# Kernel tuning notes

Measured on AMD Instinct MI355X. Metric: run time of the kernel, lower is better.

## Reference

```python
import jax, jax.numpy as jnp
import numpy as np

# ---- static config (from init_kwargs) ----
SAMPLE_RATE = 2048.0
MAX_SHIFT = int(0.025 * SAMPLE_RATE)          # 51 samples
NUM_BINS = 16
FFTLENGTH = 1.0                               # chisq_kernel_length (s)
DF = 1.0 / FFTLENGTH
NUM_FREQS = int(FFTLENGTH * SAMPLE_RATE // 2 + 1)   # 1025 == rfft bins of 2048 samples
HIGHPASS = 32.0
CHISQ_PENALTY = 1.0
_freqs = np.arange(NUM_FREQS) / FFTLENGTH
MASK = _freqs >= HIGHPASS                     # static numpy bool mask

BATCH, CHANNELS, DIM = 256, 2, 2048


def setup_inputs() -> dict:
    key = jax.random.key(0)
    k1, k2 = jax.random.split(key)
    x_hat = jax.random.normal(k1, (BATCH, CHANNELS, DIM), dtype=jnp.float32)
    x = jax.random.normal(k2, (BATCH, CHANNELS, DIM), dtype=jnp.float32)
    return {"x_hat": x_hat, "x": x}


def _center(x):
    xmin = x.min(-1, keepdims=True)
    xmax = x.max(-1, keepdims=True)
    return 2 * (x - xmin) / (xmax - xmin) - 1


def _shifted_pearson(x, y, max_shift):
    # x, y: [B, C, T]; returns corr: [W, B, C] with W = 2*max_shift + 1
    b, c, t = x.shape
    num_windows = 2 * max_shift + 1
    xp = jnp.pad(x, ((0, 0), (0, 0), (max_shift, max_shift)))
    # window w, position i -> xp[..., i + w]  (same layout as torch unfold)
    idx = jnp.arange(num_windows)[:, None] + jnp.arange(t)[None, :]   # [W, T]
    xw = xp[:, :, idx]                                                # [B, C, W, T]
    xw = jnp.transpose(xw, (2, 0, 1, 3))                              # [W, B, C, T]
    xw = xw - xw.mean(-1, keepdims=True)
    yc = y - y.mean(-1, keepdims=True)
    corr = (xw * yc).sum(-1)
    norm = (xw ** 2).sum(-1) * (yc ** 2).sum(-1)
    return corr / jnp.sqrt(norm)


def _snr_integral(a, b):
    # |4 * a * conj(b) * df| cumulatively summed over frequency
    integrand = a * jnp.conj(b)
    return jnp.abs(4 * integrand * DF).cumsum(-1)


def _chisq(htilde, stilde):
    htilde = htilde[:, :, MASK]
    stilde = stilde[:, :, MASK]
    # partition frequencies by the template's own optimal-SNR integral
    si = _snr_integral(htilde, htilde)                    # [B, C, F]
    total = si[:, :, -1:]
    bins = (jnp.arange(NUM_BINS + 1, dtype=si.dtype) / NUM_BINS) * total  # [B, C, NB+1]
    search = jax.vmap(jax.vmap(lambda a, v: jnp.searchsorted(a, v, side="right")))
    edges = search(si, bins)
    edges = jnp.clip(edges, 0, si.shape[-1] - 1)
    qtilde = htilde / jnp.sqrt(total).astype(htilde.dtype)
    # SNR per bin of the normalized template against the strain
    si2 = _snr_integral(qtilde, stilde)                   # [B, C, F]
    total2 = si2[:, :, -1:]
    right = jnp.take_along_axis(si2, edges[:, :, 1:], axis=-1)
    left = jnp.take_along_axis(si2, edges[:, :, :-1], axis=-1)
    snr_per_bin = right - left                            # [B, C, NB]
    summand = (snr_per_bin - total2 / NUM_BINS) ** 2
    chisq = NUM_BINS * summand.sum(-1) / (NUM_BINS - 1)
    return total2[:, :, 0], chisq


def reference(x_hat, x):
    x_hat = _center(x_hat)
    corr = _shifted_pearson(x_hat, x, MAX_SHIFT)          # [W, B, C]
    corr = corr.max(0)                                    # [B, C]
    loss = (1 - corr) / (1 + corr)
    htilde = jnp.fft.rfft(x_hat, axis=-1) / SAMPLE_RATE   # [B, C, 1025] complex
    stilde = jnp.fft.rfft(x, axis=-1) / SAMPLE_RATE
    _, chisq = _chisq(htilde, stilde)
    chisq = chisq * CHISQ_PENALTY
    loss = loss * (1 + chisq ** 3) ** (1.0 / 6.0)
    return loss
```

## Files before the change

kernel.cpp:

```cpp
#include <hip/hip_runtime.h>
#include <math.h>

#define ROWS 512
#define DIM 2048
#define MS 51
#define NWIN 103
#define KMIN 32
#define NMASK 993
#define INVS (1.0f/8192.0f)

__global__ __launch_bounds__(512) void fused_mfl_kernel(
    const float* __restrict__ xhat, const float* __restrict__ x,
    float* __restrict__ out)
{
    const int r = blockIdx.x;
    const int t = threadIdx.x;
    const int lane = t & 63;
    const int wave = t >> 6;
    const float* xh = xhat + (size_t)r * DIM;
    const float* xr = x + (size_t)r * DIM;

    __shared__ float smem[11780];
    float2* A  = (float2*)smem;
    float2* Bb = (float2*)(smem + 4096);
    float2* TW = (float2*)(smem + 8192);
    float* red6  = smem;
    float* siA   = smem + 9216;
    float* siBr  = smem + 10240;
    float* headS = smem + 11264;
    float* headQ = smem + 11316;
    float* tailS = smem + 11368;
    float* tailQ = smem + 11420;
    float* yhH   = smem + 11472;
    float* yhT   = smem + 11523;
    float* ycH   = smem + 11574;
    float* ycT   = smem + 11625;
    float* corrv = smem + 11676;

    __shared__ float sc[8];
    __shared__ int   edges[17];
    __shared__ float summ[16];
    __shared__ float wsA[8], wsB[8];

    float4 a4 = ((const float4*)xh)[t];
    float4 b4 = ((const float4*)xr)[t];
    float av[4] = {a4.x, a4.y, a4.z, a4.w};
    float bv[4] = {b4.x, b4.y, b4.z, b4.w};

    {
        float swv, cwv;
        sincosf((float)t * (-3.14159265358979323846f / 1024.0f), &swv, &cwv);
        TW[t] = make_float2(cwv, swv);
    }

    auto fft_stage = [&](const float2* Sp, float2* Dp, const int s) {
        const int q = t;
        const int u = q & ~(s - 1);
        float2 x0 = Sp[q];
        float2 x1 = Sp[q + 512];
        float2 x2 = Sp[q + 1024];
        float2 x3 = Sp[q + 1536];
        float t0r = x0.x + x2.x, t0i = x0.y + x2.y;
        float t1r = x0.x - x2.x, t1i = x0.y - x2.y;
        float t2r = x1.x + x3.x, t2i = x1.y + x3.y;
        float d3r = x1.x - x3.x, d3i = x1.y - x3.y;
        float t3r = d3i, t3i = -d3r;
        float2 w1 = TW[u];
        float w2r = w1.x * w1.x - w1.y * w1.y, w2i = 2.f * w1.x * w1.y;
        float w3r = w2r * w1.x - w2i * w1.y,  w3i = w2r * w1.y + w2i * w1.x;
        float y0r = t0r + t2r, y0i = t0i + t2i;
        float a1r = t1r + t3r, a1i = t1i + t3i;
        float y1r = a1r * w1.x - a1i * w1.y, y1i = a1r * w1.y + a1i * w1.x;
        float a2r = t0r - t2r, a2i = t0i - t2i;
        float y2r = a2r * w2r - a2i * w2i, y2i = a2r * w2i + a2i * w2r;
        float a3r = t1r - t3r, a3i = t1i - t3i;
        float y3r = a3r * w3r - a3i * w3i, y3i = a3r * w3i + a3i * w3r;
        int base = q + 3 * u;
        Dp[base]         = make_float2(y0r, y0i);
        Dp[base + s]     = make_float2(y1r, y1i);
        Dp[base + 2 * s] = make_float2(y2r, y2i);
        Dp[base + 3 * s] = make_float2(y3r, y3i);
    };

    {
        float mn4 = fminf(fminf(av[0], av[1]), fminf(av[2], av[3]));
        float mx4 = fmaxf(fmaxf(av[0], av[1]), fmaxf(av[2], av[3]));
        float sa = (av[0] + av[1]) + (av[2] + av[3]);
        float qa = (av[0]*av[0] + av[1]*av[1]) + (av[2]*av[2] + av[3]*av[3]);
        float sx = (bv[0] + bv[1]) + (bv[2] + bv[3]);
        float qx = (bv[0]*bv[0] + bv[1]*bv[1]) + (bv[2]*bv[2] + bv[3]*bv[3]);
        red6[t]        = mn4;
        red6[512 + t]  = mx4;
        red6[1024 + t] = sa;
        red6[1536 + t] = qa;
        red6[2048 + t] = sx;
        red6[2560 + t] = qx;
    }
    __syncthreads();
    if (wave == 0) {
        float4 u, v;
        u = ((const float4*)(red6       ))[2*lane]; v = ((const float4*)(red6       ))[2*lane+1];
        float pmn = fminf(fminf(fminf(u.x,u.y),fminf(u.z,u.w)),
                          fminf(fminf(v.x,v.y),fminf(v.z,v.w)));
        u = ((const float4*)(red6 +  512))[2*lane]; v = ((const float4*)(red6 +  512))[2*lane+1];
        float pmx = fmaxf(fmaxf(fmaxf(u.x,u.y),fmaxf(u.z,u.w)),
                          fmaxf(fmaxf(v.x,v.y),fmaxf(v.z,v.w)));
        u = ((const float4*)(red6 + 1024))[2*lane]; v = ((const float4*)(red6 + 1024))[2*lane+1];
        float psa = ((u.x+u.y)+(u.z+u.w)) + ((v.x+v.y)+(v.z+v.w));
        u = ((const float4*)(red6 + 1536))[2*lane]; v = ((const float4*)(red6 + 1536))[2*lane+1];
        float pqa = ((u.x+u.y)+(u.z+u.w)) + ((v.x+v.y)+(v.z+v.w));
        u = ((const float4*)(red6 + 2048))[2*lane]; v = ((const float4*)(red6 + 2048))[2*lane+1];
        float psx = ((u.x+u.y)+(u.z+u.w)) + ((v.x+v.y)+(v.z+v.w));
        u = ((const float4*)(red6 + 2560))[2*lane]; v = ((const float4*)(red6 + 2560))[2*lane+1];
        float pqx = ((u.x+u.y)+(u.z+u.w)) + ((v.x+v.y)+(v.z+v.w));
#pragma unroll
        for (int d = 32; d; d >>= 1) {
            pmn = fminf(pmn, __shfl_down(pmn, d));
            pmx = fmaxf(pmx, __shfl_down(pmx, d));
            psa += __shfl_down(psa, d);
            pqa += __shfl_down(pqa, d);
            psx += __shfl_down(psx, d);
            pqx += __shfl_down(pqx, d);
        }
        if (lane == 0) {
            float mn = pmn, mx = pmx;
            float scl = 2.0f / (mx - mn);
            float mean = psx * (1.0f / DIM);
            float Sm = psa - (float)DIM * mn;
            float S1v = scl * Sm - (float)DIM;
            float S2v = scl * scl * (pqa - 2.f * mn * psa + (float)DIM * mn * mn)
                      - 2.f * scl * Sm + (float)DIM;
            float Syyv = pqx - (float)DIM * mean * mean;
            sc[0] = mn; sc[1] = scl; sc[2] = mean;
            sc[3] = S1v; sc[4] = S2v; sc[5] = Syyv;
        }
    }
    __syncthreads();
    const float mnv = sc[0], scl = sc[1], mean = sc[2];
    const float S1 = sc[3], S2 = sc[4], Syy = sc[5];

#pragma unroll
    for (int j = 0; j < 4; ++j) {
        int i = 4 * t + j;
        float y = (av[j] - mnv) * scl - 1.0f;
        float z = bv[j] - mean;
        A[i] = make_float2(y, bv[j]);
        if (i < MS)        { yhH[i] = y;        ycH[i] = z; }
        if (i >= DIM - MS) { yhT[i - (DIM - MS)] = y; ycT[i - (DIM - MS)] = z; }
    }
    __syncthreads();

    if (wave < 2) {
        float v = 0.f;
        if (lane >= 1 && lane <= MS)
            v = (wave == 0) ? yhH[lane - 1] : yhT[MS - lane];
        float s = v, q = v * v;
#pragma unroll
        for (int d = 1; d < 64; d <<= 1) {
            float ys = __shfl_up(s, d);
            float yq = __shfl_up(q, d);
            if (lane >= d) { s += ys; q += yq; }
        }
        if (lane <= MS) {
            if (wave == 0) { headS[lane] = s; headQ[lane] = q; }
            else           { tailS[lane] = s; tailQ[lane] = q; }
        }
    }

    fft_stage(A, Bb, 1);    __syncthreads();
    fft_stage(Bb, A, 4);    __syncthreads();
    fft_stage(A, Bb, 16);   __syncthreads();
    fft_stage(Bb, A, 64);   __syncthreads();
    fft_stage(A, Bb, 256);  __syncthreads();

    const float MSC = 0.5f * (1.0f / 2048.0f);
    float h[2], sg[2];
#pragma unroll
    for (int j = 0; j < 2; ++j) {
        int m = 2 * t + j;
        if (m < NMASK) {
            int f = m + KMIN;
            float zfr, zfi;
            if (f < 1024) {
                float2 p = Bb[f], q2 = Bb[f + 1024];
                zfr = p.x + q2.x; zfi = p.y + q2.y;
            } else {
                float2 p = Bb[0], q2 = Bb[1024];
                zfr = p.x - q2.x; zfi = p.y - q2.y;
            }
            int g = 2048 - f;
            float2 p2 = Bb[g - 1024], q3 = Bb[g];
            float zgr = p2.x - q3.x, zgi = p2.y - q3.y;
            float hre = zfr + zgr, him = zfi - zgi;
            float sre = zfi + zgi, sim = zgr - zfr;
            h[j]  = sqrtf(hre * hre + him * him) * MSC;
            sg[j] = sqrtf(sre * sre + sim * sim) * MSC;
            float pr = hre * sre + him * sim;
            float pi = him * sre - hre * sim;
            A[f] = make_float2(pr, -pi);
            if (f < 1024) A[2048 - f] = make_float2(pr, pi);
        } else { h[j] = 0.f; sg[j] = 0.f; }
    }
    if (t < 32) {
        if (t == 0) A[0] = make_float2(0.f, 0.f);
        else {
            int f = t;
            float2 p = Bb[f], q2 = Bb[f + 1024];
            float zfr = p.x + q2.x, zfi = p.y + q2.y;
            float2 p2 = Bb[1024 - f], q3 = Bb[2048 - f];
            float zgr = p2.x - q3.x, zgi = p2.y - q3.y;
            float hre = zfr + zgr, him = zfi - zgi;
            float sre = zfi + zgi, sim = zgr - zfr;
            float pr = hre * sre + him * sim;
            float pi = him * sre - hre * sim;
            A[f] = make_float2(pr, -pi);
            A[2048 - f] = make_float2(pr, pi);
        }
    }
    __syncthreads();

    float e0 = 4.f * h[0] * h[0];
    float e1 = e0 + 4.f * h[1] * h[1];
    float g0 = 4.f * h[0] * sg[0];
    float g1 = g0 + 4.f * h[1] * sg[1];
    float totE = e1, totG = g1;
    float incE = totE, incG = totG;
#pragma unroll
    for (int d = 1; d < 64; d <<= 1) {
        float yE = __shfl_up(incE, d);
        float yG = __shfl_up(incG, d);
        if (lane >= d) { incE += yE; incG += yG; }
    }
    if (lane == 63) { wsA[wave] = incE; wsB[wave] = incG; }
    fft_stage(A, Bb, 1);
    __syncthreads();

    {
        float offE = 0.f, offG = 0.f;
        for (int w = 0; w < wave; ++w) { offE += wsA[w]; offG += wsB[w]; }
        float preE = offE + incE - totE;
        float preG = offG + incG - totG;
        siA[2 * t]      = preE + e0;
        siA[2 * t + 1]  = preE + e1;
        siBr[2 * t]     = preG + g0;
        siBr[2 * t + 1] = preG + g1;
    }
    fft_stage(Bb, A, 4);
    __syncthreads();

    const float total  = siA[NMASK - 1];
    const float qf     = 1.0f / sqrtf(total);
    const float total2 = siBr[NMASK - 1] * qf;
    if (t < 17) {
        float bin = ((float)t * (1.0f / 16.0f)) * total;
        int lo = 0, hi = NMASK;
        while (lo < hi) {
            int mid = (lo + hi) >> 1;
            if (siA[mid] <= bin) lo = mid + 1; else hi = mid;
        }
        edges[t] = (lo < NMASK - 1) ? lo : (NMASK - 1);
    }
    fft_stage(A, Bb, 16);
    __syncthreads();

    if (t < 16) {
        float snr = (siBr[edges[t + 1]] - siBr[edges[t]]) * qf;
        float d = snr - total2 * (1.0f / 16.0f);
        summ[t] = d * d;
    }
    fft_stage(Bb, A, 64);
    __syncthreads();

    fft_stage(A, Bb, 256);
    __syncthreads();

    if (t < 4 * NWIN) {
        int c = t >> 2, k = t & 3;
        int off = c - MS;
        float acc = 0.f;
        if (off > 0) {
            for (int j = k; j < off; j += 4) acc += yhH[j] * ycT[MS - off + j];
        } else if (off < 0) {
            for (int j = k; j < -off; j += 4) acc += yhT[MS + off + j] * ycH[j];
        }
        acc += __shfl_down(acc, 1);
        acc += __shfl_down(acc, 2);
        if (k == 0) {
            int sidx = (off >= 0) ? off : (2048 + off);
            float cc = (sidx < 1024) ? (Bb[sidx].x + Bb[sidx + 1024].x)
                                     : (Bb[sidx - 1024].x - Bb[sidx].x);
            float num = cc * INVS - acc;
            float sw, qw;
            if (off >= 0) { sw = S1 - headS[off];  qw = S2 - headQ[off]; }
            else          { sw = S1 - tailS[-off]; qw = S2 - tailQ[-off]; }
            float varw = qw - sw * sw * (1.0f / DIM);
            corrv[c] = num / sqrtf(varw * Syy);
        }
    }
    __syncthreads();

    if (wave == 0) {
        float m = (lane < NWIN) ? corrv[lane] : -2.0f;
        if (lane + 64 < NWIN) m = fmaxf(m, corrv[lane + 64]);
#pragma unroll
        for (int d = 32; d; d >>= 1) m = fmaxf(m, __shfl_down(m, d));
        if (lane == 0) {
            float loss0 = (1.0f - m) / (1.0f + m);
            float ssum = 0.f;
            for (int i = 0; i < 16; ++i) ssum += summ[i];
            float chisq = 16.0f * ssum / 15.0f;
            float c3 = chisq * chisq * chisq;
            out[r] = loss0 * powf(1.0f + c3, 1.0f / 6.0f);
        }
    }
}

extern "C" void kernel_launch(void* const* d_in, const int* in_sizes, int n_in,
                              void* d_out, int out_size, void* d_ws, size_t ws_size,
                              hipStream_t stream) {
    const float* xhat = (const float*)d_in[0];
    const float* x    = (const float*)d_in[1];
    float* out = (float*)d_out;
    (void)in_sizes; (void)n_in; (void)out_size; (void)d_ws; (void)ws_size;

    fused_mfl_kernel<<<ROWS, 512, 0, stream>>>(xhat, x, out);
}
```

Measured before the change: 68.43 us.

## Run forward FFT on raw inputs and use half-size inverse FFT for real correlation

The forward FFT now runs on the raw x_hat/x values rather than the centered signal. The min/max scaling is folded algebraically into the correlation numerator and window variance, which removes a barrier and the centering pass before the FFT. The inverse FFT of the real cross-spectrum is replaced by a 1024-point complex FFT on 256 threads, using a packed real-output trick. The remaining 256 threads do the SNR prefix scans and binning concurrently. This cuts FFT work and overlaps the chisq bookkeeping, at the cost of more intricate algebra with possible precision differences and idle threads during the half-size stages.

After: 67.72 us. Within noise of the previous version (-1.0%).

```diff
diff --git a/kernel.cpp b/kernel.cpp
--- a/kernel.cpp
+++ b/kernel.cpp
@@ -7,7 +7,6 @@
 #define NWIN 103
 #define KMIN 32
 #define NMASK 993
-#define INVS (1.0f/8192.0f)
 
 __global__ __launch_bounds__(512) void fused_mfl_kernel(
     const float* __restrict__ xhat, const float* __restrict__ x,
@@ -17,33 +16,37 @@
     const int t = threadIdx.x;
     const int lane = t & 63;
     const int wave = t >> 6;
-    const float* xh = xhat + (size_t)r * DIM;
-    const float* xr = x + (size_t)r * DIM;
-
-    __shared__ float smem[11780];
-    float2* A  = (float2*)smem;
-    float2* Bb = (float2*)(smem + 4096);
-    float2* TW = (float2*)(smem + 8192);
-    float* red6  = smem;
-    float* siA   = smem + 9216;
-    float* siBr  = smem + 10240;
-    float* headS = smem + 11264;
-    float* headQ = smem + 11316;
-    float* tailS = smem + 11368;
-    float* tailQ = smem + 11420;
-    float* yhH   = smem + 11472;
-    float* yhT   = smem + 11523;
-    float* ycH   = smem + 11574;
-    float* ycT   = smem + 11625;
-    float* corrv = smem + 11676;
+
+    __shared__ float smem[12928];
+    float2* A2  = (float2*)smem;
+    float2* B2  = (float2*)(smem + 4096);
+    float2* TW  = (float2*)(smem + 8192);
+    float* eArr = smem + 9216;
+    float* gArr = smem + 10240;
+    float* red6 = smem + 9216;
+    float* ah   = smem + 12288;
+    float* xhd  = smem + 12339;
+    float* at_  = smem + 12390;
+    float* xt_  = smem + 12441;
+    float* Ah   = smem + 12492;
+    float* Aqh  = smem + 12544;
+    float* Xh   = smem + 12596;
+    float* At   = smem + 12648;
+    float* Aqt  = smem + 12700;
+    float* Xt   = smem + 12752;
+    float* corrv= smem + 12804;
+    float* siA  = smem;
+    float* siBr = smem + 1024;
 
     __shared__ float sc[8];
     __shared__ int   edges[17];
     __shared__ float summ[16];
-    __shared__ float wsA[8], wsB[8];
-
-    float4 a4 = ((const float4*)xh)[t];
-    float4 b4 = ((const float4*)xr)[t];
+    __shared__ float wsA[4], wsB[4];
+
+    const float* xhp = xhat + (size_t)r * DIM;
+    const float* xrp = x    + (size_t)r * DIM;
+    float4 a4 = ((const float4*)xhp)[t];
+    float4 b4 = ((const float4*)xrp)[t];
     float av[4] = {a4.x, a4.y, a4.z, a4.w};
     float bv[4] = {b4.x, b4.y, b4.z, b4.w};
 
@@ -53,225 +56,270 @@
         TW[t] = make_float2(cwv, swv);
     }
 
-    auto fft_stage = [&](const float2* Sp, float2* Dp, const int s) {
+#pragma unroll
+    for (int j = 0; j < 4; ++j) {
+        int i = 4 * t + j;
+        A2[i] = make_float2(av[j], bv[j]);
+        if (i < MS)        { ah[i] = av[j]; xhd[i] = bv[j]; }
+        if (i >= DIM - MS) { at_[i-(DIM-MS)] = av[j]; xt_[i-(DIM-MS)] = bv[j]; }
+    }
+    {
+        float mn4 = fminf(fminf(av[0],av[1]), fminf(av[2],av[3]));
+        float mx4 = fmaxf(fmaxf(av[0],av[1]), fmaxf(av[2],av[3]));
+        float sa = (av[0]+av[1])+(av[2]+av[3]);
+        float qa = (av[0]*av[0]+av[1]*av[1])+(av[2]*av[2]+av[3]*av[3]);
+        float sx = (bv[0]+bv[1])+(bv[2]+bv[3]);
+        float qx = (bv[0]*bv[0]+bv[1]*bv[1])+(bv[2]*bv[2]+bv[3]*bv[3]);
+        red6[t] = mn4; red6[512+t] = mx4; red6[1024+t] = sa;
+        red6[1536+t] = qa; red6[2048+t] = sx; red6[2560+t] = qx;
+    }
+    __syncthreads();
+
+    auto fft2048 = [&](const float2* Sp, float2* Dp, const int s) {
         const int q = t;
         const int u = q & ~(s - 1);
-        float2 x0 = Sp[q];
-        float2 x1 = Sp[q + 512];
-        float2 x2 = Sp[q + 1024];
-        float2 x3 = Sp[q + 1536];
-        float t0r = x0.x + x2.x, t0i = x0.y + x2.y;
-        float t1r = x0.x - x2.x, t1i = x0.y - x2.y;
-        float t2r = x1.x + x3.x, t2i = x1.y + x3.y;
-        float d3r = x1.x - x3.x, d3i = x1.y - x3.y;
-        float t3r = d3i, t3i = -d3r;
+        float2 x0 = Sp[q], x1 = Sp[q+512], x2 = Sp[q+1024], x3 = Sp[q+1536];
+        float t0r=x0.x+x2.x, t0i=x0.y+x2.y;
+        float t1r=x0.x-x2.x, t1i=x0.y-x2.y;
+        float t2r=x1.x+x3.x, t2i=x1.y+x3.y;
+        float d3r=x1.x-x3.x, d3i=x1.y-x3.y;
+        float t3r=d3i, t3i=-d3r;
         float2 w1 = TW[u];
-        float w2r = w1.x * w1.x - w1.y * w1.y, w2i = 2.f * w1.x * w1.y;
-        float w3r = w2r * w1.x - w2i * w1.y,  w3i = w2r * w1.y + w2i * w1.x;
-        float y0r = t0r + t2r, y0i = t0i + t2i;
-        float a1r = t1r + t3r, a1i = t1i + t3i;
-        float y1r = a1r * w1.x - a1i * w1.y, y1i = a1r * w1.y + a1i * w1.x;
-        float a2r = t0r - t2r, a2i = t0i - t2i;
-        float y2r = a2r * w2r - a2i * w2i, y2i = a2r * w2i + a2i * w2r;
-        float a3r = t1r - t3r, a3i = t1i - t3i;
-        float y3r = a3r * w3r - a3i * w3i, y3i = a3r * w3i + a3i * w3r;
-        int base = q + 3 * u;
-        Dp[base]         = make_float2(y0r, y0i);
-        Dp[base + s]     = make_float2(y1r, y1i);
-        Dp[base + 2 * s] = make_float2(y2r, y2i);
-        Dp[base + 3 * s] = make_float2(y3r, y3i);
+        float w2r=w1.x*w1.x-w1.y*w1.y, w2i=2.f*w1.x*w1.y;
+        float w3r=w2r*w1.x-w2i*w1.y,  w3i=w2r*w1.y+w2i*w1.x;
+        float y0r=t0r+t2r, y0i=t0i+t2i;
+        float a1r=t1r+t3r, a1i=t1i+t3i;
+        float y1r=a1r*w1.x-a1i*w1.y, y1i=a1r*w1.y+a1i*w1.x;
+        float a2r=t0r-t2r, a2i=t0i-t2i;
+        float y2r=a2r*w2r-a2i*w2i, y2i=a2r*w2i+a2i*w2r;
+        float a3r=t1r-t3r, a3i=t1i-t3i;
+        float y3r=a3r*w3r-a3i*w3i, y3i=a3r*w3i+a3i*w3r;
+        int base = q + 3*u;
+        Dp[base]       = make_float2(y0r,y0i);
+        Dp[base+s]     = make_float2(y1r,y1i);
+        Dp[base+2*s]   = make_float2(y2r,y2i);
+        Dp[base+3*s]   = make_float2(y3r,y3i);
     };
-
-    {
-        float mn4 = fminf(fminf(av[0], av[1]), fminf(av[2], av[3]));
-        float mx4 = fmaxf(fmaxf(av[0], av[1]), fmaxf(av[2], av[3]));
-        float sa = (av[0] + av[1]) + (av[2] + av[3]);
-        float qa = (av[0]*av[0] + av[1]*av[1]) + (av[2]*av[2] + av[3]*av[3]);
-        float sx = (bv[0] + bv[1]) + (bv[2] + bv[3]);
-        float qx = (bv[0]*bv[0] + bv[1]*bv[1]) + (bv[2]*bv[2] + bv[3]*bv[3]);
-        red6[t]        = mn4;
-        red6[512 + t]  = mx4;
-        red6[1024 + t] = sa;
-        red6[1536 + t] = qa;
-        red6[2048 + t] = sx;
-        red6[2560 + t] = qx;
-    }
-    __syncthreads();
+    auto fft1024 = [&](const float2* Sp, float2* Dp, const int s) {
+        const int q = t;
+        const int u = q & ~(s - 1);
+        float2 x0 = Sp[q], x1 = Sp[q+256], x2 = Sp[q+512], x3 = Sp[q+768];
+        float t0r=x0.x+x2.x, t0i=x0.y+x2.y;
+        float t1r=x0.x-x2.x, t1i=x0.y-x2.y;
+        float t2r=x1.x+x3.x, t2i=x1.y+x3.y;
+        float d3r=x1.x-x3.x, d3i=x1.y-x3.y;
+        float t3r=d3i, t3i=-d3r;
+        float2 w1 = TW[2*u];
+        float w2r=w1.x*w1.x-w1.y*w1.y, w2i=2.f*w1.x*w1.y;
+        float w3r=w2r*w1.x-w2i*w1.y,  w3i=w2r*w1.y+w2i*w1.x;
+        float y0r=t0r+t2r, y0i=t0i+t2i;
+        float a1r=t1r+t3r, a1i=t1i+t3i;
+        float y1r=a1r*w1.x-a1i*w1.y, y1i=a1r*w1.y+a1i*w1.x;
+        float a2r=t0r-t2r, a2i=t0i-t2i;
+        float y2r=a2r*w2r-a2i*w2i, y2i=a2r*w2i+a2i*w2r;
+        float a3r=t1r-t3r, a3i=t1i-t3i;
+        float y3r=a3r*w3r-a3i*w3i, y3i=a3r*w3i+a3i*w3r;
+        int base = q + 3*u;
+        Dp[base]       = make_float2(y0r,y0i);
+        Dp[base+s]     = make_float2(y1r,y1i);
+        Dp[base+2*s]   = make_float2(y2r,y2i);
+        Dp[base+3*s]   = make_float2(y3r,y3i);
+    };
+
+    fft2048(A2, B2, 1);
     if (wave == 0) {
         float4 u, v;
-        u = ((const float4*)(red6       ))[2*lane]; v = ((const float4*)(red6       ))[2*lane+1];
-        float pmn = fminf(fminf(fminf(u.x,u.y),fminf(u.z,u.w)),
-                          fminf(fminf(v.x,v.y),fminf(v.z,v.w)));
-        u = ((const float4*)(red6 +  512))[2*lane]; v = ((const float4*)(red6 +  512))[2*lane+1];
-        float pmx = fmaxf(fmaxf(fmaxf(u.x,u.y),fmaxf(u.z,u.w)),
-                          fmaxf(fmaxf(v.x,v.y),fmaxf(v.z,v.w)));
-        u = ((const float4*)(red6 + 1024))[2*lane]; v = ((const float4*)(red6 + 1024))[2*lane+1];
-        float psa = ((u.x+u.y)+(u.z+u.w)) + ((v.x+v.y)+(v.z+v.w));
-        u = ((const float4*)(red6 + 1536))[2*lane]; v = ((const float4*)(red6 + 1536))[2*lane+1];
-        float pqa = ((u.x+u.y)+(u.z+u.w)) + ((v.x+v.y)+(v.z+v.w));
-        u = ((const float4*)(red6 + 2048))[2*lane]; v = ((const float4*)(red6 + 2048))[2*lane+1];
-        float psx = ((u.x+u.y)+(u.z+u.w)) + ((v.x+v.y)+(v.z+v.w));
-        u = ((const float4*)(red6 + 2560))[2*lane]; v = ((const float4*)(red6 + 2560))[2*lane+1];
-        float pqx = ((u.x+u.y)+(u.z+u.w)) + ((v.x+v.y)+(v.z+v.w));
+        u=((const float4*)(red6     ))[2*lane]; v=((const float4*)(red6     ))[2*lane+1];
+        float pmn=fminf(fminf(fminf(u.x,u.y),fminf(u.z,u.w)),fminf(fminf(v.x,v.y),fminf(v.z,v.w)));
+        u=((const float4*)(red6+ 512))[2*lane]; v=((const float4*)(red6+ 512))[2*lane+1];
+        float pmx=fmaxf(fmaxf(fmaxf(u.x,u.y),fmaxf(u.z,u.w)),fmaxf(fmaxf(v.x,v.y),fmaxf(v.z,v.w)));
+        u=((const float4*)(red6+1024))[2*lane]; v=((const float4*)(red6+1024))[2*lane+1];
+        float psa=((u.x+u.y)+(u.z+u.w))+((v.x+v.y)+(v.z+v.w));
+        u=((const float4*)(red6+1536))[2*lane]; v=((const float4*)(red6+1536))[2*lane+1];
+        float pqa=((u.x+u.y)+(u.z+u.w))+((v.x+v.y)+(v.z+v.w));
+        u=((const float4*)(red6+2048))[2*lane]; v=((const float4*)(red6+2048))[2*lane+1];
+        float psx=((u.x+u.y)+(u.z+u.w))+((v.x+v.y)+(v.z+v.w));
+        u=((const float4*)(red6+2560))[2*lane]; v=((const float4*)(red6+2560))[2*lane+1];
+        float pqx=((u.x+u.y)+(u.z+u.w))+((v.x+v.y)+(v.z+v.w));
 #pragma unroll
         for (int d = 32; d; d >>= 1) {
-            pmn = fminf(pmn, __shfl_down(pmn, d));
-            pmx = fmaxf(pmx, __shfl_down(pmx, d));
-            psa += __shfl_down(psa, d);
-            pqa += __shfl_down(pqa, d);
-            psx += __shfl_down(psx, d);
-            pqx += __shfl_down(pqx, d);
+            pmn=fminf(pmn,__shfl_down(pmn,d)); pmx=fmaxf(pmx,__shfl_down(pmx,d));
+            psa+=__shfl_down(psa,d); pqa+=__shfl_down(pqa,d);
+            psx+=__shfl_down(psx,d); pqx+=__shfl_down(pqx,d);
         }
         if (lane == 0) {
-            float mn = pmn, mx = pmx;
-            float scl = 2.0f / (mx - mn);
-            float mean = psx * (1.0f / DIM);
-            float Sm = psa - (float)DIM * mn;
-            float S1v = scl * Sm - (float)DIM;
-            float S2v = scl * scl * (pqa - 2.f * mn * psa + (float)DIM * mn * mn)
-                      - 2.f * scl * Sm + (float)DIM;
-            float Syyv = pqx - (float)DIM * mean * mean;
-            sc[0] = mn; sc[1] = scl; sc[2] = mean;
-            sc[3] = S1v; sc[4] = S2v; sc[5] = Syyv;
-        }
-    }
-    __syncthreads();
-    const float mnv = sc[0], scl = sc[1], mean = sc[2];
-    const float S1 = sc[3], S2 = sc[4], Syy = sc[5];
-
-#pragma unroll
-    for (int j = 0; j < 4; ++j) {
-        int i = 4 * t + j;
-        float y = (av[j] - mnv) * scl - 1.0f;
-        float z = bv[j] - mean;
-        A[i] = make_float2(y, bv[j]);
-        if (i < MS)        { yhH[i] = y;        ycH[i] = z; }
-        if (i >= DIM - MS) { yhT[i - (DIM - MS)] = y; ycT[i - (DIM - MS)] = z; }
-    }
-    __syncthreads();
-
-    if (wave < 2) {
-        float v = 0.f;
-        if (lane >= 1 && lane <= MS)
-            v = (wave == 0) ? yhH[lane - 1] : yhT[MS - lane];
-        float s = v, q = v * v;
+            float scl = 2.0f/(pmx - pmn);
+            float Cc  = scl*pmn + 1.0f;
+            float mean = psx * (1.0f/DIM);
+            sc[0]=scl; sc[1]=Cc; sc[2]=mean; sc[3]=psa; sc[4]=pqa;
+            sc[5]=pqx - (float)DIM*mean*mean;
+        }
+    }
+    __syncthreads();
+
+    fft2048(B2, A2, 4);
+    if (wave == 2) {
+        float va=0.f, vq=0.f, vx=0.f;
+        if (lane >= 1 && lane <= MS) { float aa=ah[lane-1]; va=aa; vq=aa*aa; vx=xhd[lane-1]; }
 #pragma unroll
         for (int d = 1; d < 64; d <<= 1) {
-            float ys = __shfl_up(s, d);
-            float yq = __shfl_up(q, d);
-            if (lane >= d) { s += ys; q += yq; }
-        }
-        if (lane <= MS) {
-            if (wave == 0) { headS[lane] = s; headQ[lane] = q; }
-            else           { tailS[lane] = s; tailQ[lane] = q; }
-        }
-    }
-
-    fft_stage(A, Bb, 1);    __syncthreads();
-    fft_stage(Bb, A, 4);    __syncthreads();
-    fft_stage(A, Bb, 16);   __syncthreads();
-    fft_stage(Bb, A, 64);   __syncthreads();
-    fft_stage(A, Bb, 256);  __syncthreads();
+            float ya=__shfl_up(va,d), yq=__shfl_up(vq,d), yx=__shfl_up(vx,d);
+            if (lane >= d) { va+=ya; vq+=yq; vx+=yx; }
+        }
+        if (lane <= MS) { Ah[lane]=va; Aqh[lane]=vq; Xh[lane]=vx; }
+    } else if (wave == 3) {
+        float va=0.f, vq=0.f, vx=0.f;
+        if (lane >= 1 && lane <= MS) { float aa=at_[MS-lane]; va=aa; vq=aa*aa; vx=xt_[MS-lane]; }
+#pragma unroll
+        for (int d = 1; d < 64; d <<= 1) {
+            float ya=__shfl_up(va,d), yq=__shfl_up(vq,d), yx=__shfl_up(vx,d);
+            if (lane >= d) { va+=ya; vq+=yq; vx+=yx; }
+        }
+        if (lane <= MS) { At[lane]=va; Aqt[lane]=vq; Xt[lane]=vx; }
+    }
+    __syncthreads();
+    fft2048(A2, B2, 16);  __syncthreads();
+    fft2048(B2, A2, 64);  __syncthreads();
+    fft2048(A2, B2, 256); __syncthreads();
+
+    const float scl = sc[0], Cc = sc[1], mean = sc[2];
+    const float Sa = sc[3], Qa = sc[4], Szz = sc[5];
 
     const float MSC = 0.5f * (1.0f / 2048.0f);
-    float h[2], sg[2];
 #pragma unroll
     for (int j = 0; j < 2; ++j) {
         int m = 2 * t + j;
+        float e = 0.f, g = 0.f;
         if (m < NMASK) {
             int f = m + KMIN;
             float zfr, zfi;
-            if (f < 1024) {
-                float2 p = Bb[f], q2 = Bb[f + 1024];
-                zfr = p.x + q2.x; zfi = p.y + q2.y;
-            } else {
-                float2 p = Bb[0], q2 = Bb[1024];
-                zfr = p.x - q2.x; zfi = p.y - q2.y;
-            }
-            int g = 2048 - f;
-            float2 p2 = Bb[g - 1024], q3 = Bb[g];
+            if (f < 1024) { float2 p=B2[f], q2=B2[f+1024]; zfr=p.x+q2.x; zfi=p.y+q2.y; }
+            else          { float2 p=B2[0], q2=B2[1024];   zfr=p.x-q2.x; zfi=p.y-q2.y; }
+            int gi = 2048 - f;
+            float2 p2 = B2[gi-1024], q3 = B2[gi];
             float zgr = p2.x - q3.x, zgi = p2.y - q3.y;
             float hre = zfr + zgr, him = zfi - zgi;
             float sre = zfi + zgi, sim = zgr - zfr;
-            h[j]  = sqrtf(hre * hre + him * him) * MSC;
-            sg[j] = sqrtf(sre * sre + sim * sim) * MSC;
-            float pr = hre * sre + him * sim;
-            float pi = him * sre - hre * sim;
-            A[f] = make_float2(pr, -pi);
-            if (f < 1024) A[2048 - f] = make_float2(pr, pi);
-        } else { h[j] = 0.f; sg[j] = 0.f; }
+            float hm = scl * sqrtf(hre*hre + him*him) * MSC;
+            float sm = sqrtf(sre*sre + sim*sim) * MSC;
+            e = 4.f*hm*hm; g = 4.f*hm*sm;
+            float pr = hre*sre + him*sim;
+            float pi = him*sre - hre*sim;
+            A2[f] = make_float2(pr, -pi);
+            if (f < 1024) A2[2048-f] = make_float2(pr, pi);
+        }
+        eArr[m] = e; gArr[m] = g;
     }
     if (t < 32) {
-        if (t == 0) A[0] = make_float2(0.f, 0.f);
+        if (t == 0) A2[0] = make_float2(0.f, 0.f);
         else {
             int f = t;
-            float2 p = Bb[f], q2 = Bb[f + 1024];
-            float zfr = p.x + q2.x, zfi = p.y + q2.y;
-            float2 p2 = Bb[1024 - f], q3 = Bb[2048 - f];
-            float zgr = p2.x - q3.x, zgi = p2.y - q3.y;
-            float hre = zfr + zgr, him = zfi - zgi;
-            float sre = zfi + zgi, sim = zgr - zfr;
-            float pr = hre * sre + him * sim;
-            float pi = him * sre - hre * sim;
-            A[f] = make_float2(pr, -pi);
-            A[2048 - f] = make_float2(pr, pi);
-        }
-    }
-    __syncthreads();
-
-    float e0 = 4.f * h[0] * h[0];
-    float e1 = e0 + 4.f * h[1] * h[1];
-    float g0 = 4.f * h[0] * sg[0];
-    float g1 = g0 + 4.f * h[1] * sg[1];
-    float totE = e1, totG = g1;
-    float incE = totE, incG = totG;
-#pragma unroll
-    for (int d = 1; d < 64; d <<= 1) {
-        float yE = __shfl_up(incE, d);
-        float yG = __shfl_up(incG, d);
-        if (lane >= d) { incE += yE; incG += yG; }
-    }
-    if (lane == 63) { wsA[wave] = incE; wsB[wave] = incG; }
-    fft_stage(A, Bb, 1);
-    __syncthreads();
-
-    {
-        float offE = 0.f, offG = 0.f;
-        for (int w = 0; w < wave; ++w) { offE += wsA[w]; offG += wsB[w]; }
+            float2 p=B2[f], q2=B2[f+1024];
+            float zfr=p.x+q2.x, zfi=p.y+q2.y;
+            float2 p2=B2[1024-f], q3=B2[2048-f];
+            float zgr=p2.x-q3.x, zgi=p2.y-q3.y;
+            float hre=zfr+zgr, him=zfi-zgi;
+            float sre=zfi+zgi, sim=zgr-zfr;
+            float pr=hre*sre+him*sim, pi=him*sre-hre*sim;
+            A2[f]=make_float2(pr,-pi);
+            A2[2048-f]=make_float2(pr,pi);
+        }
+    }
+    __syncthreads();
+
+    float2* Qlo = B2;
+    float2* Qhi = B2 + 1024;
+
+    float se0=0,se1=0,se2=0,se3=0, sg0=0,sg1=0,sg2=0,sg3=0;
+    float incE=0, incG=0, totE=0, totG=0;
+
+    if (t < 256) {
+        const int q = t;
+        float2 wA = TW[q], wB = TW[q+256];
+        auto mkQ = [&](int k, float2 w, int ni) -> float2 {
+            float2 Pa = A2[k], Pb = A2[k+1024];
+            float D1r = Pa.x+Pb.x, D1i = Pa.y+Pb.y;
+            float D2r = Pa.x-Pb.x, D2i = Pa.y-Pb.y;
+            float Er = D2r*w.x - D2i*w.y;
+            float Ei = D2r*w.y + D2i*w.x;
+            if (ni) return make_float2(D1r - Er, D1i - Ei);
+            return make_float2(D1r + Ei, D1i - Er);
+        };
+        float2 x0 = mkQ(q,     wA, 0);
+        float2 x1 = mkQ(q+256, wB, 0);
+        float2 x2 = mkQ(q+512, wA, 1);
+        float2 x3 = mkQ(q+768, wB, 1);
+        float t0r=x0.x+x2.x, t0i=x0.y+x2.y;
+        float t1r=x0.x-x2.x, t1i=x0.y-x2.y;
+        float t2r=x1.x+x3.x, t2i=x1.y+x3.y;
+        float d3r=x1.x-x3.x, d3i=x1.y-x3.y;
+        float t3r=d3i, t3i=-d3r;
+        float2 w1 = TW[2*q];
+        float w2r=w1.x*w1.x-w1.y*w1.y, w2i=2.f*w1.x*w1.y;
+        float w3r=w2r*w1.x-w2i*w1.y,  w3i=w2r*w1.y+w2i*w1.x;
+        float y0r=t0r+t2r, y0i=t0i+t2i;
+        float a1r=t1r+t3r, a1i=t1i+t3i;
+        float y1r=a1r*w1.x-a1i*w1.y, y1i=a1r*w1.y+a1i*w1.x;
+        float a2r=t0r-t2r, a2i=t0i-t2i;
+        float y2r=a2r*w2r-a2i*w2i, y2i=a2r*w2i+a2i*w2r;
+        float a3r=t1r-t3r, a3i=t1i-t3i;
+        float y3r=a3r*w3r-a3i*w3i, y3i=a3r*w3i+a3i*w3r;
+        Qlo[4*q]   = make_float2(y0r,y0i);
+        Qlo[4*q+1] = make_float2(y1r,y1i);
+        Qlo[4*q+2] = make_float2(y2r,y2i);
+        Qlo[4*q+3] = make_float2(y3r,y3i);
+    } else {
+        int tt = t - 256;
+        float4 e4 = ((const float4*)eArr)[tt];
+        float4 g4 = ((const float4*)gArr)[tt];
+        se0=e4.x; se1=se0+e4.y; se2=se1+e4.z; se3=se2+e4.w;
+        sg0=g4.x; sg1=sg0+g4.y; sg2=sg1+g4.z; sg3=sg2+g4.w;
+        totE=se3; totG=sg3; incE=totE; incG=totG;
+#pragma unroll
+        for (int d = 1; d < 64; d <<= 1) {
+            float yE=__shfl_up(incE,d), yG=__shfl_up(incG,d);
+            if (lane >= d) { incE+=yE; incG+=yG; }
+        }
+        if (lane == 63) { wsA[wave-4]=incE; wsB[wave-4]=incG; }
+    }
+    __syncthreads();
+
+    if (t < 256) { fft1024(Qlo, Qhi, 4); }
+    else {
+        int tt = t - 256, w4 = wave - 4;
+        float offE=0.f, offG=0.f;
+        for (int w = 0; w < w4; ++w) { offE+=wsA[w]; offG+=wsB[w]; }
         float preE = offE + incE - totE;
         float preG = offG + incG - totG;
-        siA[2 * t]      = preE + e0;
-        siA[2 * t + 1]  = preE + e1;
-        siBr[2 * t]     = preG + g0;
-        siBr[2 * t + 1] = preG + g1;
-    }
-    fft_stage(Bb, A, 4);
-    __syncthreads();
-
-    const float total  = siA[NMASK - 1];
-    const float qf     = 1.0f / sqrtf(total);
-    const float total2 = siBr[NMASK - 1] * qf;
-    if (t < 17) {
-        float bin = ((float)t * (1.0f / 16.0f)) * total;
+        ((float4*)siA)[tt]  = make_float4(preE+se0, preE+se1, preE+se2, preE+se3);
+        ((float4*)siBr)[tt] = make_float4(preG+sg0, preG+sg1, preG+sg2, preG+sg3);
+    }
+    __syncthreads();
+
+    if (t < 256) { fft1024(Qhi, Qlo, 16); }
+    else if (t < 256 + 17) {
+        int tl = t - 256;
+        float total = siA[NMASK-1];
+        float bin = ((float)tl * (1.0f/16.0f)) * total;
         int lo = 0, hi = NMASK;
-        while (lo < hi) {
-            int mid = (lo + hi) >> 1;
-            if (siA[mid] <= bin) lo = mid + 1; else hi = mid;
-        }
-        edges[t] = (lo < NMASK - 1) ? lo : (NMASK - 1);
-    }
-    fft_stage(A, Bb, 16);
-    __syncthreads();
-
-    if (t < 16) {
-        float snr = (siBr[edges[t + 1]] - siBr[edges[t]]) * qf;
-        float d = snr - total2 * (1.0f / 16.0f);
-        summ[t] = d * d;
-    }
-    fft_stage(Bb, A, 64);
-    __syncthreads();
-
-    fft_stage(A, Bb, 256);
+        while (lo < hi) { int mid=(lo+hi)>>1; if (siA[mid] <= bin) lo=mid+1; else hi=mid; }
+        edges[tl] = (lo < NMASK-1) ? lo : (NMASK-1);
+    }
+    __syncthreads();
+
+    if (t < 256) { fft1024(Qlo, Qhi, 64); }
+    else if (t < 256 + 16) {
+        int tl = t - 256;
+        float total = siA[NMASK-1];
+        float qf = 1.0f / sqrtf(total);
+        float total2 = siBr[NMASK-1] * qf;
+        float snr = (siBr[edges[tl+1]] - siBr[edges[tl]]) * qf;
+        float d = snr - total2 * (1.0f/16.0f);
+        summ[tl] = d * d;
+    }
+    __syncthreads();
+
+    if (t < 256) { fft1024(Qhi, Qlo, 256); }
     __syncthreads();
 
     if (t < 4 * NWIN) {
@@ -279,38 +327,48 @@
         int off = c - MS;
         float acc = 0.f;
         if (off > 0) {
-            for (int j = k; j < off; j += 4) acc += yhH[j] * ycT[MS - off + j];
+            for (int j = k; j < off; j += 4) acc += ah[j] * (xt_[MS-off+j] - mean);
         } else if (off < 0) {
-            for (int j = k; j < -off; j += 4) acc += yhT[MS + off + j] * ycH[j];
+            int o = -off;
+            for (int j = k; j < o; j += 4) acc += at_[MS-o+j] * (xhd[j] - mean);
         }
         acc += __shfl_down(acc, 1);
         acc += __shfl_down(acc, 2);
         if (k == 0) {
             int sidx = (off >= 0) ? off : (2048 + off);
-            float cc = (sidx < 1024) ? (Bb[sidx].x + Bb[sidx + 1024].x)
-                                     : (Bb[sidx - 1024].x - Bb[sidx].x);
-            float num = cc * INVS - acc;
-            float sw, qw;
-            if (off >= 0) { sw = S1 - headS[off];  qw = S2 - headQ[off]; }
-            else          { sw = S1 - tailS[-off]; qw = S2 - tailQ[-off]; }
-            float varw = qw - sw * sw * (1.0f / DIM);
-            corrv[c] = num / sqrtf(varw * Syy);
+            float2 Fv = Qlo[sidx >> 1];
+            float val = (sidx & 1) ? -Fv.y : Fv.x;
+            float circ = val * (1.0f/8192.0f);
+            float Sin_a, Sin_q, Zex, nin;
+            if (off >= 0) {
+                Sin_a = Sa - Ah[off]; Sin_q = Qa - Aqh[off];
+                Zex = Xt[off] - (float)off * mean; nin = 2048.0f - (float)off;
+            } else {
+                int o = -off;
+                Sin_a = Sa - At[o]; Sin_q = Qa - Aqt[o];
+                Zex = Xh[o] - (float)o * mean; nin = 2048.0f - (float)o;
+            }
+            float num = scl * (circ - acc) + Cc * Zex;
+            float Sw  = scl * Sin_a - Cc * nin;
+            float Sw2 = scl*scl*Sin_q - 2.f*scl*Cc*Sin_a + Cc*Cc*nin;
+            float varw = Sw2 - Sw * Sw * (1.0f/2048.0f);
+            corrv[c] = num / sqrtf(varw * Szz);
         }
     }
     __syncthreads();
 
     if (wave == 0) {
-        float m = (lane < NWIN) ? corrv[lane] : -2.0f;
+        float m = corrv[lane];
         if (lane + 64 < NWIN) m = fmaxf(m, corrv[lane + 64]);
 #pragma unroll
         for (int d = 32; d; d >>= 1) m = fmaxf(m, __shfl_down(m, d));
         if (lane == 0) {
             float loss0 = (1.0f - m) / (1.0f + m);
-            float ssum = 0.f;
-            for (int i = 0; i < 16; ++i) ssum += summ[i];
-            float chisq = 16.0f * ssum / 15.0f;
+            float ss = 0.f;
+            for (int i = 0; i < 16; ++i) ss += summ[i];
+            float chisq = 16.0f * ss / 15.0f;
             float c3 = chisq * chisq * chisq;
-            out[r] = loss0 * powf(1.0f + c3, 1.0f / 6.0f);
+            out[r] = loss0 * powf(1.0f + c3, 1.0f/6.0f);
         }
     }
 }
```
